# Performance work log

Hardware: AMD Instinct MI355X
Metric: run time of the kernel (lower is better)

The kernel has to match this reference:

```python
import jax, jax.numpy as jnp
import numpy as np

D = 128
H = 4
B = 4096
K = 64
N_USERS = 200000
BISECT_ITERS = 50


def l2norm(x, axis=-1, eps=1e-12):
    n = jnp.linalg.norm(x, axis=axis, keepdims=True)
    return x / jnp.maximum(n, eps)


def entmax_bisect(x, alpha, n_iter=BISECT_ITERS):
    # x, alpha: [B, K, 1]; entmax normalization over the neighbor axis (axis=1)
    # p = max((alpha-1)*x - tau, 0)**(1/(alpha-1)) with tau found by bisection so sum_k p = 1
    am1 = alpha - 1.0            # in (0,1) since alpha = sigmoid(.)+1
    q = 1.0 / am1                # exponent > 1, so p is smooth at 0
    xs = x * am1
    mx = jnp.max(xs, axis=1, keepdims=True)
    tau_lo = mx - 1.0            # f(tau_lo) >= 0
    tau_hi = mx                  # f(tau_hi) <= 0

    def p_of(tau):
        t = jnp.maximum(xs - tau, 0.0)
        safe = jnp.where(t > 0.0, t, 1.0)
        return jnp.where(t > 0.0, safe ** q, 0.0)

    def body(i, carry):
        lo, hi = carry
        mid = 0.5 * (lo + hi)
        f_m = jnp.sum(p_of(mid), axis=1, keepdims=True) - 1.0
        lo = jnp.where(f_m >= 0.0, mid, lo)
        hi = jnp.where(f_m >= 0.0, hi, mid)
        return (lo, hi)

    tau_lo, tau_hi = jax.lax.fori_loop(0, n_iter, body, (tau_lo, tau_hi))
    p = p_of(0.5 * (tau_lo + tau_hi))
    return p / jnp.sum(p, axis=1, keepdims=True)


def batchnorm(x, g, b, eps=1e-5):
    # training-mode BatchNorm1d: batch statistics, biased variance
    m = jnp.mean(x, axis=0)
    v = jnp.mean((x - m) ** 2, axis=0)
    return (x - m) * jax.lax.rsqrt(v + eps) * g + b


def setup_inputs() -> dict:
    key = jax.random.key(0)
    ks = jax.random.split(key, 16)
    s = 0.05
    return {
        'nodes': jax.random.randint(ks[0], (B,), 0, N_USERS),
        'neighbors': jax.random.randint(ks[1], (B, K), 0, N_USERS),
        'u2e': jax.random.normal(ks[2], (N_USERS, D), jnp.float32),
        'att1_w': jax.random.normal(ks[3], (H, 2 * D, D), jnp.float32) * s,
        'att1_b': jnp.zeros((H, D), jnp.float32),
        'att2_w': jax.random.normal(ks[4], (H, D, D // 4), jnp.float32) * s,
        'att2_b': jnp.zeros((H, D // 4), jnp.float32),
        'att3_w': jax.random.normal(ks[5], (H, D // 4, 1), jnp.float32) * s,
        'att3_b': jnp.zeros((H, 1), jnp.float32),
        'lin1_w': jax.random.normal(ks[6], (H, D, 1), jnp.float32) * s,
        'lin1_b': jnp.zeros((H, 1), jnp.float32),
        'gate_w': jax.random.normal(ks[7], (3 * D, D), jnp.float32) * s,
        'gate_b': jnp.zeros((D,), jnp.float32),
        'bn_g': jnp.ones((D,), jnp.float32),
        'bn_b': jnp.zeros((D,), jnp.float32),
        'bn1_g': jnp.ones((D,), jnp.float32),
        'bn1_b': jnp.zeros((D,), jnp.float32),
        'in_w': jax.random.normal(ks[8], (D, D), jnp.float32) * s,
        'in_b': jnp.zeros((D,), jnp.float32),
        'out_w': jax.random.normal(ks[9], (D, D), jnp.float32) * s,
        'out_b': jnp.zeros((D,), jnp.float32),
    }


def reference(nodes, neighbors, u2e, att1_w, att1_b, att2_w, att2_b, att3_w,
              att3_b, lin1_w, lin1_b, gate_w, gate_b, bn_g, bn_b, bn1_g,
              bn1_b, in_w, in_b, out_w, out_b):
    n_heads = att1_w.shape[0]
    e_n = l2norm(u2e[neighbors])                     # [B,K,D] normalized neighbor embeds
    u = u2e[nodes]                                   # [B,D]
    b, k, d = e_n.shape
    feats = []
    for h in range(n_heads):
        u_n = l2norm(u)
        x = jnp.concatenate(
            [e_n, jnp.broadcast_to(u_n[:, None, :], (b, k, d))], axis=-1)
        alpha = jax.nn.sigmoid(e_n @ lin1_w[h] + lin1_b[h]) + 1.0  # [B,K,1]
        sc = jax.nn.selu(x @ att1_w[h] + att1_b[h])
        sc = jax.nn.selu(sc @ att2_w[h] + att2_b[h])
        sc = sc @ att3_w[h] + att3_b[h]                            # [B,K,1]
        att = entmax_bisect(sc, alpha)                             # [B,K,1]
        u = jnp.einsum('bkd,bk->bd', e_n, att[..., 0])             # weighted pool
        feats.append(u)
    att_hist = sum(feats) / n_heads                  # [B,D]
    # GAT_MLP (dropout omitted: eval)
    h1 = batchnorm(att_hist, bn_g, bn_b)
    h1 = jax.nn.selu(h1 @ in_w + in_b)
    h1 = batchnorm(h1, bn1_g, bn1_b)
    neigh = h1 @ out_w + out_b                       # [B,D]
    self_f = u2e[nodes]
    comb = jnp.concatenate([self_f, neigh, self_f * neigh], axis=-1)
    gama = jax.nn.sigmoid(comb @ gate_w + gate_b)
    return gama * self_f + (1.0 - gama) * neigh
```

## Files before the change

### kernel.cpp

```cpp
#include <hip/hip_runtime.h>
#include <stdint.h>

#define NB 4096
#define NK 64
#define ND 128
#define NH 4
#define ES 136
#define ESW (ES/2)
#define MR 16
#define GS 392
#define SFS 132

typedef __attribute__((ext_vector_type(8))) short bf16x8;
typedef __attribute__((ext_vector_type(4))) float f32x4;

__device__ __forceinline__ float seluf(float x) {
    float e = 1.6732632423543772f * (__expf(x) - 1.f);
    return 1.0507009873554805f * (x > 0.f ? x : e);
}
__device__ __forceinline__ float sigmoidf_(float x) {
    return __fdividef(1.f, 1.f + __expf(-x));
}
__device__ __forceinline__ uint32_t f2bf2(float a, float b) {
    uint32_t ua = __float_as_uint(a); ua += 0x7fffu + ((ua >> 16) & 1u);
    uint32_t ub = __float_as_uint(b); ub += 0x7fffu + ((ub >> 16) & 1u);
    return (ua >> 16) | (ub & 0xffff0000u);
}
__device__ __forceinline__ uint16_t bf1(float v) {
    uint32_t u = __float_as_uint(v); u += 0x7fffu + ((u >> 16) & 1u);
    return (uint16_t)(u >> 16);
}
__device__ __forceinline__ float bflo(uint32_t v) { return __uint_as_float(v << 16); }
__device__ __forceinline__ float bfhi(uint32_t v) { return __uint_as_float(v & 0xffff0000u); }
__device__ __forceinline__ float bf2f(uint16_t h) { return __uint_as_float(((uint32_t)h) << 16); }

__global__ __launch_bounds__(256)
void k_prep(const float* __restrict__ att1_w, const float* __restrict__ att2_w,
            const float* __restrict__ in_w, const float* __restrict__ out_w,
            const float* __restrict__ gate_w,
            uint16_t* __restrict__ wt1, uint16_t* __restrict__ wt2,
            uint16_t* __restrict__ wt_in, uint16_t* __restrict__ wt_out,
            uint16_t* __restrict__ wt_gate)
{
    const int bx = blockIdx.x;
    const int t = threadIdx.x;
    if (bx < 64) {
        const int h = bx >> 4;
        const int q = bx & 15;
        {
            int n = t >> 1, kh = t & 1;
            for (int k0 = q * 4; k0 < q * 4 + 4; ++k0) {
                int k = k0 * 2 + kh;
                float v = att1_w[(size_t)h * 32768 + (size_t)k * ND + n];
                float vo = __shfl_xor(v, 1, 64);
                if (kh == 0)
                    ((uint32_t*)wt1)[((size_t)h * ND + n) * 64 + k0] = f2bf2(v, vo);
            }
        }
        {
            int c = t & 31, dh = t >> 5;
            int d0 = q;
            int d = d0 * 8 + dh;
            float v = att2_w[(size_t)h * 4096 + (size_t)d * 32 + c];
            float vo = __shfl_xor(v, 32, 64);
            if ((dh & 1) == 0)
                ((uint32_t*)wt2)[((size_t)h * 32 + c) * 64 + d0 * 4 + (dh >> 1)] = f2bf2(v, vo);
        }
    } else if (bx < 72) {
        int n0 = (bx - 64) * 16;
        for (int n = n0; n < n0 + 16; ++n)
            for (int k = t; k < ND; k += 256)
                wt_in[n * ND + k] = bf1(in_w[(size_t)k * ND + n]);
    } else if (bx < 80) {
        int n0 = (bx - 72) * 16;
        for (int n = n0; n < n0 + 16; ++n)
            for (int k = t; k < ND; k += 256)
                wt_out[n * ND + k] = bf1(out_w[(size_t)k * ND + n]);
    } else {
        int n0 = (bx - 80) * 16;
        for (int n = n0; n < n0 + 16; ++n)
            for (int k = t; k < 384; k += 256)
                wt_gate[n * 384 + k] = bf1(gate_w[(size_t)k * ND + n]);
    }
}

__global__ __launch_bounds__(256, 4)
void k_att(const int* __restrict__ nodes, const int* __restrict__ neighbors,
           const float* __restrict__ u2e,
           const float* __restrict__ att1_w, const float* __restrict__ att1_b,
           const float* __restrict__ att2_b,
           const float* __restrict__ att3_w, const float* __restrict__ att3_b,
           const float* __restrict__ lin1_w, const float* __restrict__ lin1_b,
           const uint16_t* __restrict__ wt1, const uint16_t* __restrict__ wt2,
           float* __restrict__ hist_out,
           float* __restrict__ sums, float* __restrict__ sumsq)
{
    __shared__ alignas(16) uint16_t e_sh[NK * ES];
    __shared__ alignas(16) uint16_t s1_sh[NK * ES];
    __shared__ float u_sh[ND], up_sh[ND], hist_sh[ND];
    __shared__ float alpha_sh[NH * NK];
    __shared__ float sc_sh[NK], att_sh[NK];
    __shared__ float red_sh[512];

    const int b = blockIdx.x;
    const int t = threadIdx.x;
    const int lane = t & 63;
    const int wave = t >> 6;
    const int lh = lane & 15;
    const int lg = lane >> 4;

    for (int k = wave; k < NK; k += 4) {
        int idx = neighbors[b * NK + k];
        float2 v = ((const float2*)(u2e + (size_t)idx * ND))[lane];
        float ss = v.x * v.x + v.y * v.y;
        #pragma unroll
        for (int m = 1; m < 64; m <<= 1) ss += __shfl_xor(ss, m, 64);
        float r = 1.0f / fmaxf(sqrtf(ss), 1e-12f);
        ((uint32_t*)e_sh)[k * ESW + lane] = f2bf2(v.x * r, v.y * r);
    }
    if (t < ND) {
        u_sh[t] = u2e[(size_t)nodes[b] * ND + t];
        hist_sh[t] = 0.f;
    }
    __syncthreads();

    {
        const float* lw = lin1_w + wave * ND;
        float lb = lin1_b[wave];
        #pragma unroll
        for (int it = 0; it < 4; ++it) {
            int k = it * 16 + (lane >> 2);
            int qd = lane & 3;
            const uint32_t* er = (const uint32_t*)e_sh + k * ESW + qd * 16;
            const float* lr = lw + qd * 32;
            float ap = 0.f;
            #pragma unroll 8
            for (int j2 = 0; j2 < 16; ++j2) {
                uint32_t v = er[j2];
                ap += bflo(v) * lr[2 * j2] + bfhi(v) * lr[2 * j2 + 1];
            }
            ap += __shfl_xor(ap, 1, 64);
            ap += __shfl_xor(ap, 2, 64);
            if (qd == 0)
                alpha_sh[wave * NK + k] = sigmoidf_(ap + lb) + 1.0f;
        }
    }

    for (int h = 0; h < NH; ++h) {
        float rnorm;
        {
            float a = u_sh[lane], c = u_sh[lane + 64];
            float ss = a * a + c * c;
            #pragma unroll
            for (int m = 1; m < 64; m <<= 1) ss += __shfl_xor(ss, m, 64);
            rnorm = 1.0f / fmaxf(sqrtf(ss), 1e-12f);
        }
        {
            int d = t & 127, half = t >> 7;
            const float* wb = att1_w + (size_t)h * 32768 + (size_t)(ND + half * 64) * ND + d;
            float p = 0.f;
            #pragma unroll 8
            for (int j = 0; j < 64; ++j)
                p += u_sh[half * 64 + j] * wb[j * ND];
            red_sh[t] = p * rnorm;
        }
        __syncthreads();
        if (t < ND)
            up_sh[t] = red_sh[t] + red_sh[t + 128] + att1_b[h * ND + t];
        __syncthreads();

        {
            const uint16_t* WB = wt1 + ((size_t)h * ND + wave * 32) * ND;
            bf16x8 B[4][2];
            #pragma unroll
            for (int kk = 0; kk < 4; ++kk)
                #pragma unroll
                for (int nt = 0; nt < 2; ++nt)
                    B[kk][nt] = *(const bf16x8*)(WB + (nt * 16 + lh) * ND + kk * 32 + lg * 8);
            f32x4 z = {0.f, 0.f, 0.f, 0.f};
            f32x4 acc[4][2] = {{z, z}, {z, z}, {z, z}, {z, z}};
            #pragma unroll
            for (int mt = 0; mt < 4; ++mt) {
                #pragma unroll
                for (int kk = 0; kk < 4; ++kk) {
                    bf16x8 A = *(const bf16x8*)(e_sh + (mt * 16 + lh) * ES + kk * 32 + lg * 8);
                    acc[mt][0] = __builtin_amdgcn_mfma_f32_16x16x32_bf16(A, B[kk][0], acc[mt][0], 0, 0, 0);
                    acc[mt][1] = __builtin_amdgcn_mfma_f32_16x16x32_bf16(A, B[kk][1], acc[mt][1], 0, 0, 0);
                }
            }
            float up0 = up_sh[wave * 32 + lh];
            float up1 = up_sh[wave * 32 + 16 + lh];
            #pragma unroll
            for (int mt = 0; mt < 4; ++mt)
                #pragma unroll
                for (int nt = 0; nt < 2; ++nt) {
                    float upv = nt ? up1 : up0;
                    #pragma unroll
                    for (int r = 0; r < 4; ++r) {
                        float v = seluf(acc[mt][nt][r] + upv);
                        s1_sh[(mt * 16 + lg * 4 + r) * ES + wave * 32 + nt * 16 + lh] = bf1(v);
                    }
                }
        }
        __syncthreads();

        {
            const uint16_t* WB2 = wt2 + (size_t)h * 32 * ND;
            bf16x8 B2[4][2];
            #pragma unroll
            for (int kk = 0; kk < 4; ++kk)
                #pragma unroll
                for (int nt = 0; nt < 2; ++nt)
                    B2[kk][nt] = *(const bf16x8*)(WB2 + (nt * 16 + lh) * ND + kk * 32 + lg * 8);
            f32x4 z = {0.f, 0.f, 0.f, 0.f};
            f32x4 acc2[2] = {z, z};
            #pragma unroll
            for (int kk = 0; kk < 4; ++kk) {
                bf16x8 A = *(const bf16x8*)(s1_sh + (wave * 16 + lh) * ES + kk * 32 + lg * 8);
                acc2[0] = __builtin_amdgcn_mfma_f32_16x16x32_bf16(A, B2[kk][0], acc2[0], 0, 0, 0);
                acc2[1] = __builtin_amdgcn_mfma_f32_16x16x32_bf16(A, B2[kk][1], acc2[1], 0, 0, 0);
            }
            float w3a = att3_w[h * 32 + lh],      b2a = att2_b[h * 32 + lh];
            float w3b = att3_w[h * 32 + 16 + lh], b2b = att2_b[h * 32 + 16 + lh];
            float b3 = att3_b[h];
            #pragma unroll
            for (int r = 0; r < 4; ++r) {
                float v = seluf(acc2[0][r] + b2a) * w3a + seluf(acc2[1][r] + b2b) * w3b;
                v += __shfl_xor(v, 1, 64);
                v += __shfl_xor(v, 2, 64);
                v += __shfl_xor(v, 4, 64);
                v += __shfl_xor(v, 8, 64);
                if (lh == 0)
                    sc_sh[wave * 16 + lg * 4 + r] = v + b3;
            }
        }
        __syncthreads();

        if (wave == 0) {
            float x   = sc_sh[lane];
            float am1 = alpha_sh[h * NK + lane] - 1.0f;
            float q   = 1.0f / am1;
            float em1 = q - 1.0f;
            float xs  = x * am1;
            float mx = xs;
            #pragma unroll
            for (int m = 1; m < 64; m <<= 1) mx = fmaxf(mx, __shfl_xor(mx, m, 64));
            float tau = mx - 1.0f;
            for (int it = 0; it < 6; ++it) {
                float tt = xs - tau;
                bool pos = tt > 0.f;
                float lgn = __logf(pos ? tt : 1.f);
                float p  = pos ? __expf(q * lgn) : 0.f;
                float dp = pos ? q * __expf(em1 * lgn) : 0.f;
                float s0 = p, s1 = dp;
                #pragma unroll
                for (int m = 1; m < 64; m <<= 1) {
                    s0 += __shfl_xor(s0, m, 64);
                    s1 += __shfl_xor(s1, m, 64);
                }
                tau += __fdividef(s0 - 1.0f, fmaxf(s1, 1e-30f));
                tau = fminf(tau, mx - 1e-6f);
            }
            float tt = xs - tau;
            bool pos = tt > 0.f;
            float p = pos ? __expf(q * __logf(pos ? tt : 1.f)) : 0.f;
            float s0 = p;
            #pragma unroll
            for (int m = 1; m < 64; m <<= 1) s0 += __shfl_xor(s0, m, 64);
            att_sh[lane] = __fdividef(p, s0);
        }
        __syncthreads();

        {
            int d2 = t & 63, qk = t >> 6;
            const uint32_t* E = (const uint32_t*)e_sh;
            float px = 0.f, py = 0.f;
            #pragma unroll 8
            for (int k = qk * 16; k < qk * 16 + 16; ++k) {
                uint32_t v = E[k * ESW + d2];
                float a = att_sh[k];
                px += bflo(v) * a;
                py += bfhi(v) * a;
            }
            red_sh[qk * 128 + d2 * 2]     = px;
            red_sh[qk * 128 + d2 * 2 + 1] = py;
        }
        __syncthreads();
        if (t < ND) {
            float un = red_sh[t] + red_sh[128 + t] + red_sh[256 + t] + red_sh[384 + t];
            u_sh[t] = un;
            hist_sh[t] += un;
        }
        __syncthreads();
    }
    if (t < ND) {
        float hv = hist_sh[t] * 0.25f;
        hist_out[(size_t)b * ND + t] = hv;
        atomicAdd(&sums[t], hv);
        atomicAdd(&sumsq[t], hv * hv);
    }
}

__global__ __launch_bounds__(256)
void k_mlp1(const float* __restrict__ hist,
            const float* __restrict__ sums, const float* __restrict__ sumsq,
            const float* __restrict__ bn_g, const float* __restrict__ bn_b,
            const uint16_t* __restrict__ wt_in, const float* __restrict__ in_b,
            uint16_t* __restrict__ h1b,
            float* __restrict__ sums1, float* __restrict__ sumsq1)
{
    __shared__ alignas(16) uint16_t xh[MR * ES];
    const int t = threadIdx.x;
    const int lane = t & 63;
    const int wave = t >> 6;
    const int lh = lane & 15;
    const int lg = lane >> 4;
    const int row0 = blockIdx.x * MR;

    #pragma unroll
    for (int it = 0; it < 4; ++it) {
        int pos = t + it * 256;
        int r = pos >> 6, d2 = pos & 63;
        int d0 = d2 * 2;
        float m0 = sums[d0] * (1.f / 4096.f);
        float v0 = sumsq[d0] * (1.f / 4096.f) - m0 * m0;
        float sc0 = bn_g[d0] * rsqrtf(v0 + 1e-5f);
        float sh0 = bn_b[d0] - m0 * sc0;
        float m1 = sums[d0 + 1] * (1.f / 4096.f);
        float v1 = sumsq[d0 + 1] * (1.f / 4096.f) - m1 * m1;
        float sc1 = bn_g[d0 + 1] * rsqrtf(v1 + 1e-5f);
        float sh1 = bn_b[d0 + 1] - m1 * sc1;
        float2 hv = *(const float2*)(hist + (size_t)(row0 + r) * ND + d0);
        ((uint32_t*)xh)[r * ESW + d2] = f2bf2(hv.x * sc0 + sh0, hv.y * sc1 + sh1);
    }
    __syncthreads();

    const uint16_t* WB = wt_in + (size_t)(wave * 32) * ND;
    bf16x8 B[4][2];
    #pragma unroll
    for (int kk = 0; kk < 4; ++kk)
        #pragma unroll
        for (int nt = 0; nt < 2; ++nt)
            B[kk][nt] = *(const bf16x8*)(WB + (nt * 16 + lh) * ND + kk * 32 + lg * 8);
    f32x4 z = {0.f, 0.f, 0.f, 0.f};
    f32x4 acc[2] = {z, z};
    #pragma unroll
    for (int kk = 0; kk < 4; ++kk) {
        bf16x8 A = *(const bf16x8*)(xh + lh * ES + kk * 32 + lg * 8);
        acc[0] = __builtin_amdgcn_mfma_f32_16x16x32_bf16(A, B[kk][0], acc[0], 0, 0, 0);
        acc[1] = __builtin_amdgcn_mfma_f32_16x16x32_bf16(A, B[kk][1], acc[1], 0, 0, 0);
    }
    #pragma unroll
    for (int nt = 0; nt < 2; ++nt) {
        int col = wave * 32 + nt * 16 + lh;
        float bia = in_b[col];
        float s = 0.f, q = 0.f;
        #pragma unroll
        for (int r = 0; r < 4; ++r) {
            int row = lg * 4 + r;
            float hv = seluf(acc[nt][r] + bia);
            h1b[(size_t)(row0 + row) * ND + col] = bf1(hv);
            s += hv; q += hv * hv;
        }
        s += __shfl_xor(s, 16, 64); s += __shfl_xor(s, 32, 64);
        q += __shfl_xor(q, 16, 64); q += __shfl_xor(q, 32, 64);
        if (lg == 0) {
            atomicAdd(&sums1[col], s);
            atomicAdd(&sumsq1[col], q);
        }
    }
}

__global__ __launch_bounds__(256)
void k_final(const uint16_t* __restrict__ h1b,
             const float* __restrict__ sums1, const float* __restrict__ sumsq1,
             const float* __restrict__ bn1_g, const float* __restrict__ bn1_b,
             const uint16_t* __restrict__ wt_out, const float* __restrict__ out_b,
             const uint16_t* __restrict__ wt_gate, const float* __restrict__ gate_b,
             const int* __restrict__ nodes, const float* __restrict__ u2e,
             float* __restrict__ out)
{
    __shared__ alignas(16) uint16_t xh[MR * ES];
    __shared__ float sff[MR * SFS];
    __shared__ alignas(16) uint16_t gtile[MR * GS];
    const int t = threadIdx.x;
    const int lane = t & 63;
    const int wave = t >> 6;
    const int lh = lane & 15;
    const int lg = lane >> 4;
    const int row0 = blockIdx.x * MR;

    #pragma unroll
    for (int it = 0; it < 4; ++it) {
        int pos = t + it * 256;
        int r = pos >> 6, d2 = pos & 63;
        int d0 = d2 * 2;
        float m0 = sums1[d0] * (1.f / 4096.f);
        float v0 = sumsq1[d0] * (1.f / 4096.f) - m0 * m0;
        float sc0 = bn1_g[d0] * rsqrtf(v0 + 1e-5f);
        float sh0 = bn1_b[d0] - m0 * sc0;
        float m1 = sums1[d0 + 1] * (1.f / 4096.f);
        float v1 = sumsq1[d0 + 1] * (1.f / 4096.f) - m1 * m1;
        float sc1 = bn1_g[d0 + 1] * rsqrtf(v1 + 1e-5f);
        float sh1 = bn1_b[d0 + 1] - m1 * sc1;
        uint32_t hw = ((const uint32_t*)h1b)[(size_t)(row0 + r) * 64 + d2];
        ((uint32_t*)xh)[r * ESW + d2] = f2bf2(bflo(hw) * sc0 + sh0, bfhi(hw) * sc1 + sh1);
        float2 sv = *(const float2*)(u2e + (size_t)nodes[row0 + r] * ND + d0);
        sff[r * SFS + d0]     = sv.x;
        sff[r * SFS + d0 + 1] = sv.y;
        ((uint32_t*)gtile)[r * (GS / 2) + d2] = f2bf2(sv.x, sv.y);
    }
    __syncthreads();

    f32x4 z = {0.f, 0.f, 0.f, 0.f};
    f32x4 accN[2] = {z, z};
    {
        const uint16_t* WB = wt_out + (size_t)(wave * 32) * ND;
        bf16x8 B[4][2];
        #pragma unroll
        for (int kk = 0; kk < 4; ++kk)
            #pragma unroll
            for (int nt = 0; nt < 2; ++nt)
                B[kk][nt] = *(const bf16x8*)(WB + (nt * 16 + lh) * ND + kk * 32 + lg * 8);
        #pragma unroll
        for (int kk = 0; kk < 4; ++kk) {
            bf16x8 A = *(const bf16x8*)(xh + lh * ES + kk * 32 + lg * 8);
            accN[0] = __builtin_amdgcn_mfma_f32_16x16x32_bf16(A, B[kk][0], accN[0], 0, 0, 0);
            accN[1] = __builtin_amdgcn_mfma_f32_16x16x32_bf16(A, B[kk][1], accN[1], 0, 0, 0);
        }
    }
    #pragma unroll
    for (int nt = 0; nt < 2; ++nt) {
        int col = wave * 32 + nt * 16 + lh;
        float bia = out_b[col];
        #pragma unroll
        for (int r = 0; r < 4; ++r) {
            int row = lg * 4 + r;
            float n = accN[nt][r] + bia;
            float s = sff[row * SFS + col];
            gtile[row * GS + 128 + col] = bf1(n);
            gtile[row * GS + 256 + col] = bf1(s * n);
        }
    }
    __syncthreads();

    f32x4 accG[2] = {z, z};
    #pragma unroll
    for (int kk = 0; kk < 12; ++kk) {
        bf16x8 A = *(const bf16x8*)(gtile + lh * GS + kk * 32 + lg * 8);
        #pragma unroll
        for (int nt = 0; nt < 2; ++nt) {
            bf16x8 Bf = *(const bf16x8*)(wt_gate + (size_t)(wave * 32 + nt * 16 + lh) * 384 + kk * 32 + lg * 8);
            accG[nt] = __builtin_amdgcn_mfma_f32_16x16x32_bf16(A, Bf, accG[nt], 0, 0, 0);
        }
    }
    #pragma unroll
    for (int nt = 0; nt < 2; ++nt) {
        int col = wave * 32 + nt * 16 + lh;
        float gb = gate_b[col];
        float ob = out_b[col];
        #pragma unroll
        for (int r = 0; r < 4; ++r) {
            int row = lg * 4 + r;
            float gama = sigmoidf_(accG[nt][r] + gb);
            float s = sff[row * SFS + col];
            float n = accN[nt][r] + ob;
            out[(size_t)(row0 + row) * ND + col] = gama * s + (1.f - gama) * n;
        }
    }
}

extern "C" void kernel_launch(void* const* d_in, const int* in_sizes, int n_in,
                              void* d_out, int out_size, void* d_ws, size_t ws_size,
                              hipStream_t stream)
{
    const int*   nodes     = (const int*)d_in[0];
    const int*   neighbors = (const int*)d_in[1];
    const float* u2e       = (const float*)d_in[2];
    const float* att1_w    = (const float*)d_in[3];
    const float* att1_b    = (const float*)d_in[4];
    const float* att2_w    = (const float*)d_in[5];
    const float* att2_b    = (const float*)d_in[6];
    const float* att3_w    = (const float*)d_in[7];
    const float* att3_b    = (const float*)d_in[8];
    const float* lin1_w    = (const float*)d_in[9];
    const float* lin1_b    = (const float*)d_in[10];
    const float* gate_w    = (const float*)d_in[11];
    const float* gate_b    = (const float*)d_in[12];
    const float* bn_g      = (const float*)d_in[13];
    const float* bn_b      = (const float*)d_in[14];
    const float* bn1_g     = (const float*)d_in[15];
    const float* bn1_b     = (const float*)d_in[16];
    const float* in_w      = (const float*)d_in[17];
    const float* in_b      = (const float*)d_in[18];
    const float* out_w     = (const float*)d_in[19];
    const float* out_b     = (const float*)d_in[20];
    float* out = (float*)d_out;

    float* ws      = (float*)d_ws;
    float* g_hist  = ws;
    float* st      = ws + (size_t)NB * ND;
    uint16_t* wt1  = (uint16_t*)(st + 512);
    uint16_t* wt2  = wt1 + (size_t)NH * ND * ND;
    uint16_t* wt_in   = wt2 + (size_t)NH * 32 * ND;
    uint16_t* wt_out  = wt_in + (size_t)ND * ND;
    uint16_t* wt_gate = wt_out + (size_t)ND * ND;
    uint16_t* h1b     = wt_gate + (size_t)ND * 384;

    (void)hipMemsetAsync(st, 0, 512 * sizeof(float), stream);

    k_prep<<<88, 256, 0, stream>>>(att1_w, att2_w, in_w, out_w, gate_w,
                                   wt1, wt2, wt_in, wt_out, wt_gate);
    k_att<<<NB, 256, 0, stream>>>(nodes, neighbors, u2e,
                                  att1_w, att1_b, att2_b,
                                  att3_w, att3_b, lin1_w, lin1_b,
                                  wt1, wt2,
                                  g_hist, st, st + 128);
    k_mlp1<<<NB / MR, 256, 0, stream>>>(g_hist, st, st + 128, bn_g, bn_b,
                                        wt_in, in_b, h1b, st + 256, st + 384);
    k_final<<<NB / MR, 256, 0, stream>>>(h1b, st + 256, st + 384, bn1_g, bn1_b,
                                         wt_out, out_b, wt_gate, gate_b,
                                         nodes, u2e, out);
}
```

Measured before the change: 526.0 us.

## Replicate per-head u/attention state per wave to drop block barriers

Each wave now holds its own copy of the pooled user vector in registers and a per-wave shared slot. Each wave computes its slice of the att1 user projection, the entmax solve, and the full weighted pool redundantly, so several __syncthreads and shared reductions per head are removed. This trades redundant ALU work: all four waves run the Newton entmax loop, and each pools over all 64 neighbours instead of a quarter. The aim is to cut barrier stalls and the serial single-wave entmax phase in the attention kernel.

```diff
diff --git a/kernel.cpp b/kernel.cpp
--- a/kernel.cpp
+++ b/kernel.cpp
@@ -32,7 +32,6 @@
 }
 __device__ __forceinline__ float bflo(uint32_t v) { return __uint_as_float(v << 16); }
 __device__ __forceinline__ float bfhi(uint32_t v) { return __uint_as_float(v & 0xffff0000u); }
-__device__ __forceinline__ float bf2f(uint16_t h) { return __uint_as_float(((uint32_t)h) << 16); }
 
 __global__ __launch_bounds__(256)
 void k_prep(const float* __restrict__ att1_w, const float* __restrict__ att2_w,
@@ -97,10 +96,10 @@
 {
     __shared__ alignas(16) uint16_t e_sh[NK * ES];
     __shared__ alignas(16) uint16_t s1_sh[NK * ES];
-    __shared__ float u_sh[ND], up_sh[ND], hist_sh[ND];
     __shared__ float alpha_sh[NH * NK];
-    __shared__ float sc_sh[NK], att_sh[NK];
-    __shared__ float red_sh[512];
+    __shared__ float sc_sh[NK];
+    __shared__ float att_str[4 * NK];
+    __shared__ float u_str[4 * ND];
 
     const int b = blockIdx.x;
     const int t = threadIdx.x;
@@ -118,10 +117,10 @@
         float r = 1.0f / fmaxf(sqrtf(ss), 1e-12f);
         ((uint32_t*)e_sh)[k * ESW + lane] = f2bf2(v.x * r, v.y * r);
     }
-    if (t < ND) {
-        u_sh[t] = u2e[(size_t)nodes[b] * ND + t];
-        hist_sh[t] = 0.f;
-    }
+    float2 uv = ((const float2*)(u2e + (size_t)nodes[b] * ND))[lane];
+    float px = uv.x, py = uv.y;
+    ((float2*)(u_str + wave * ND))[lane] = uv;
+    float hx = 0.f, hy = 0.f;
     __syncthreads();
 
     {
@@ -149,25 +148,26 @@
     for (int h = 0; h < NH; ++h) {
         float rnorm;
         {
-            float a = u_sh[lane], c = u_sh[lane + 64];
-            float ss = a * a + c * c;
+            float ss = px * px + py * py;
             #pragma unroll
             for (int m = 1; m < 64; m <<= 1) ss += __shfl_xor(ss, m, 64);
             rnorm = 1.0f / fmaxf(sqrtf(ss), 1e-12f);
         }
-        {
-            int d = t & 127, half = t >> 7;
-            const float* wb = att1_w + (size_t)h * 32768 + (size_t)(ND + half * 64) * ND + d;
+        float up0, up1;
+        {
+            int dl = lane & 31, jh = lane >> 5;
+            const float* wb = att1_w + (size_t)h * 32768
+                            + (size_t)(ND + jh * 64) * ND + wave * 32 + dl;
+            const float* us = u_str + wave * ND + jh * 64;
             float p = 0.f;
             #pragma unroll 8
             for (int j = 0; j < 64; ++j)
-                p += u_sh[half * 64 + j] * wb[j * ND];
-            red_sh[t] = p * rnorm;
-        }
-        __syncthreads();
-        if (t < ND)
-            up_sh[t] = red_sh[t] + red_sh[t + 128] + att1_b[h * ND + t];
-        __syncthreads();
+                p += us[j] * wb[(size_t)j * ND];
+            p += __shfl_xor(p, 32, 64);
+            float upfull = p * rnorm + att1_b[h * ND + wave * 32 + dl];
+            up0 = __shfl(upfull, lh, 64);
+            up1 = __shfl(upfull, lh + 16, 64);
+        }
 
         {
             const uint16_t* WB = wt1 + ((size_t)h * ND + wave * 32) * ND;
@@ -188,8 +188,6 @@
                     acc[mt][1] = __builtin_amdgcn_mfma_f32_16x16x32_bf16(A, B[kk][1], acc[mt][1], 0, 0, 0);
                 }
             }
-            float up0 = up_sh[wave * 32 + lh];
-            float up1 = up_sh[wave * 32 + 16 + lh];
             #pragma unroll
             for (int mt = 0; mt < 4; ++mt)
                 #pragma unroll
@@ -236,7 +234,7 @@
         }
         __syncthreads();
 
-        if (wave == 0) {
+        {
             float x   = sc_sh[lane];
             float am1 = alpha_sh[h * NK + lane] - 1.0f;
             float q   = 1.0f / am1;
@@ -267,37 +265,32 @@
             float s0 = p;
             #pragma unroll
             for (int m = 1; m < 64; m <<= 1) s0 += __shfl_xor(s0, m, 64);
-            att_sh[lane] = __fdividef(p, s0);
-        }
-        __syncthreads();
-
-        {
-            int d2 = t & 63, qk = t >> 6;
+            att_str[wave * NK + lane] = __fdividef(p, s0);
+        }
+
+        {
             const uint32_t* E = (const uint32_t*)e_sh;
-            float px = 0.f, py = 0.f;
+            const float* as = att_str + wave * NK;
+            float nx = 0.f, ny = 0.f;
             #pragma unroll 8
-            for (int k = qk * 16; k < qk * 16 + 16; ++k) {
-                uint32_t v = E[k * ESW + d2];
-                float a = att_sh[k];
-                px += bflo(v) * a;
-                py += bfhi(v) * a;
-            }
-            red_sh[qk * 128 + d2 * 2]     = px;
-            red_sh[qk * 128 + d2 * 2 + 1] = py;
-        }
-        __syncthreads();
-        if (t < ND) {
-            float un = red_sh[t] + red_sh[128 + t] + red_sh[256 + t] + red_sh[384 + t];
-            u_sh[t] = un;
-            hist_sh[t] += un;
-        }
-        __syncthreads();
-    }
-    if (t < ND) {
-        float hv = hist_sh[t] * 0.25f;
-        hist_out[(size_t)b * ND + t] = hv;
-        atomicAdd(&sums[t], hv);
-        atomicAdd(&sumsq[t], hv * hv);
+            for (int k = 0; k < NK; ++k) {
+                uint32_t v = E[k * ESW + lane];
+                float a = as[k];
+                nx += bflo(v) * a;
+                ny += bfhi(v) * a;
+            }
+            px = nx; py = ny;
+            ((float2*)(u_str + wave * ND))[lane] = make_float2(px, py);
+            hx += px; hy += py;
+        }
+    }
+    if (wave == 0) {
+        float hvx = hx * 0.25f, hvy = hy * 0.25f;
+        ((float2*)(hist_out + (size_t)b * ND))[lane] = make_float2(hvx, hvy);
+        atomicAdd(&sums[2 * lane], hvx);
+        atomicAdd(&sums[2 * lane + 1], hvy);
+        atomicAdd(&sumsq[2 * lane], hvx * hvx);
+        atomicAdd(&sumsq[2 * lane + 1], hvy * hvy);
     }
 }
 
```

Measured after the change: 590.0 us. 1.12x slower.
